# Kernel tuning notes

Measured on AMD Instinct MI355X. Metric: run time of the kernel, lower is better.

## Reference

```python
import jax, jax.numpy as jnp
import numpy as np

N_NODES = 8192
GNN_DIM = 512
N_FEAT = 64
N_ITER = 4


def setup_inputs() -> dict:
    key = jax.random.key(0)
    ks = jax.random.split(key, 8)
    scale = 1.0 / np.sqrt(GNN_DIM)
    return {
        "labels": jax.random.normal(ks[0], (N_NODES, GNN_DIM), dtype=jnp.float32),
        "adj": jax.random.uniform(ks[1], (N_NODES, N_NODES), dtype=jnp.float32),
        "features": jax.random.normal(ks[2], (N_FEAT,), dtype=jnp.float32),
        "W_self": jax.random.normal(ks[3], (GNN_DIM, GNN_DIM), dtype=jnp.float32) * scale,
        "b_self": jax.random.normal(ks[4], (GNN_DIM,), dtype=jnp.float32) * scale,
        "W_neigh": jax.random.normal(ks[5], (GNN_DIM, GNN_DIM), dtype=jnp.float32) * scale,
        "W_fc": jax.random.normal(ks[6], (1, GNN_DIM + N_FEAT), dtype=jnp.float32) * scale,
        "b_fc": jax.random.normal(ks[7], (1,), dtype=jnp.float32) * scale,
    }


def reference(labels, adj, features, W_self, b_self, W_neigh, W_fc, b_fc):
    x = labels  # [N, D]
    for _ in range(N_ITER):
        acc = adj @ x                                   # [N, D] neighbor aggregation
        x = jax.nn.relu(x @ W_self.T + b_self + acc @ W_neigh.T)
    pooled = jnp.mean(x, axis=0)                        # [D]
    z = jnp.concatenate([pooled, features]) @ W_fc.T + b_fc  # [1]
    return jax.nn.sigmoid(z)
```

## Files before the change

kernel.cpp:

```cpp
#include <hip/hip_runtime.h>

typedef __bf16 bf16;
typedef bf16 bf16x8 __attribute__((ext_vector_type(8)));
typedef bf16 bf16x4 __attribute__((ext_vector_type(4)));
typedef float f32x4 __attribute__((ext_vector_type(4)));
typedef long longx2 __attribute__((ext_vector_type(2)));
typedef unsigned int u32;
typedef unsigned int u32x2 __attribute__((ext_vector_type(2)));
typedef unsigned char u8;
typedef unsigned long long u64;

constexpr int NN = 8192;
constexpr int DD = 512;
constexpr size_t PSZB = (size_t)NN * DD * 2;
constexpr size_t PSZE = (size_t)NN * DD;
constexpr int NS = 4;

static __device__ inline bf16x8 cvt8(const float* __restrict__ p) {
  f32x4 a = *(const f32x4*)p;
  f32x4 b = *(const f32x4*)(p + 4);
  bf16x8 r;
  r[0] = (bf16)a[0]; r[1] = (bf16)a[1]; r[2] = (bf16)a[2]; r[3] = (bf16)a[3];
  r[4] = (bf16)b[0]; r[5] = (bf16)b[1]; r[6] = (bf16)b[2]; r[7] = (bf16)b[3];
  return r;
}

static __device__ inline unsigned f32_to_e4m3(float x) {
  float a = fabsf(x);
  unsigned s = (__float_as_uint(x) >> 24) & 0x80u;
  if (!(a < 448.f)) a = 448.f;
  if (a < 0.015625f)
    return s | (unsigned)(int)__builtin_rintf(a * 512.f);
  int e = (int)((__float_as_uint(a) >> 23) & 0xFF) - 127;
  float mul = __uint_as_float((unsigned)(130 - e) << 23);
  int t = (int)__builtin_rintf(a * mul);
  return s | (unsigned)((e + 6) * 8 + t);
}

#define GLDS(g, l) __builtin_amdgcn_global_load_lds( \
    (const __attribute__((address_space(1))) unsigned int*)(const void*)(g), \
    (__attribute__((address_space(3))) unsigned int*)(void*)(l), 16, 0, 0)


__global__ __launch_bounds__(256) void convert_w_kernel(
    const float* __restrict__ a, const float* __restrict__ b,
    bf16* __restrict__ ao, bf16* __restrict__ bo, float* __restrict__ pooled) {
  int tid = (int)threadIdx.x;
  if (blockIdx.x == 0) {
    pooled[tid] = 0.f;
    pooled[tid + 256] = 0.f;
  }
  int i8 = ((int)blockIdx.x * 256 + tid) * 8;
  if (i8 < DD * DD) {
    *(bf16x8*)&ao[i8] = cvt8(a + i8);
  } else {
    int j = i8 - DD * DD;
    *(bf16x8*)&bo[j] = cvt8(b + j);
  }
}

__global__ __launch_bounds__(256) void convert_adj_kernel(
    const float* __restrict__ a, u8* __restrict__ o) {
  int i = (int)blockIdx.x * 256 + (int)threadIdx.x;
  int row  = i >> 10;
  int rem  = i & 1023;
  int g    = rem >> 3;
  int fq   = rem & 3;
  int h    = (rem >> 2) & 1;
  const float* p = a + (size_t)row * NN + g * 64 + h * 32 + fq * 8;
  f32x4 v0 = *(const f32x4*)p;
  f32x4 v1 = *(const f32x4*)(p + 4);
  u32 w0 = 0, w1 = 0;
  w0 = __builtin_amdgcn_cvt_pk_fp8_f32(v0[0], v0[1], w0, false);
  w0 = __builtin_amdgcn_cvt_pk_fp8_f32(v0[2], v0[3], w0, true);
  w1 = __builtin_amdgcn_cvt_pk_fp8_f32(v1[0], v1[1], w1, false);
  w1 = __builtin_amdgcn_cvt_pk_fp8_f32(v1[2], v1[3], w1, true);
  u32x2 w; w[0] = w0; w[1] = w1;
  *(u32x2*)(o + (size_t)row * NN + g * 64 + fq * 16 + h * 8) = w;
}

__global__ __launch_bounds__(256) void convert_x_kernel(
    const float* __restrict__ src, bf16* __restrict__ xb, u8* __restrict__ xbT8) {
  __shared__ __align__(16) float tile[64][68];
  const int tid = (int)threadIdx.x;
  const int r0 = (int)blockIdx.x * 64;
  const int c0 = (int)blockIdx.y * 64;
#pragma unroll
  for (int p = 0; p < 4; ++p) {
    int row = p * 16 + (tid >> 4);
    int col = (tid & 15) * 4;
    *(f32x4*)&tile[row][col] = *(const f32x4*)&src[(size_t)(r0 + row) * DD + c0 + col];
  }
  __syncthreads();
#pragma unroll
  for (int p = 0; p < 4; ++p) {
    int row = p * 16 + (tid >> 4);
    int col = (tid & 15) * 4;
    f32x4 v = *(const f32x4*)&tile[row][col];
    bf16x4 o;
    o[0] = (bf16)v[0]; o[1] = (bf16)v[1]; o[2] = (bf16)v[2]; o[3] = (bf16)v[3];
    *(bf16x4*)&xb[(size_t)(r0 + row) * DD + c0 + col] = o;
  }
  {
    int c = tid >> 2;
    int rp = (tid & 3) * 16;
    size_t base = (size_t)(c0 + c) * NN + r0;
#pragma unroll
    for (int b = 0; b < 2; ++b) {
      u32 lo = 0, hi = 0;
      lo = __builtin_amdgcn_cvt_pk_fp8_f32(tile[rp + 8 * b + 0][c], tile[rp + 8 * b + 1][c], lo, false);
      lo = __builtin_amdgcn_cvt_pk_fp8_f32(tile[rp + 8 * b + 2][c], tile[rp + 8 * b + 3][c], lo, true);
      hi = __builtin_amdgcn_cvt_pk_fp8_f32(tile[rp + 8 * b + 4][c], tile[rp + 8 * b + 5][c], hi, false);
      hi = __builtin_amdgcn_cvt_pk_fp8_f32(tile[rp + 8 * b + 6][c], tile[rp + 8 * b + 7][c], hi, true);
      int u = (rp >> 3) + b;
      u32x2 w; w[0] = lo; w[1] = hi;
      *(u32x2*)&xbT8[base + (u & 3) * 16 + (u >> 2) * 8] = w;
    }
  }
}


__device__ __forceinline__ void stage_half8(const u8* __restrict__ g, int grow0, int k0b,
                                            u8* smbase, int wave, int lane) {
  int row = grow0 + wave * 16 + (lane >> 2);
  int col = k0b + (((lane & 3) ^ ((lane >> 2) & 3)) << 4);
  GLDS(g + (size_t)row * NN + col, smbase + wave * 1024);
}

__global__ __launch_bounds__(512, 2)
void gemm1_kernel(const u8* __restrict__ adjb, const u8* __restrict__ xbT8,
                  bf16* __restrict__ pbase) {
  __shared__ __align__(16) u8 sm[65536];
  const int bid  = (int)blockIdx.x;
  const int xcd  = bid & 7, ii = bid >> 3;
  const int cb   = ii & 1;
  const int jj_  = xcd + 8 * (ii >> 1);
  const int p    = jj_ >> 2;
  const int s    = jj_ & 3;
  const int prow0 = p * 256;
  const int bcol0 = cb * 256;
  const int kb    = s * 2048;
  bf16* __restrict__ P = pbase + (size_t)s * PSZE;

  const int tid  = (int)threadIdx.x;
  const int lane = tid & 63;
  const int wave = tid >> 6;
  const int wr   = wave >> 2;
  const int wc   = wave & 3;
  const int fr   = lane & 15, fq = lane >> 4;

  f32x4 acc[8][4] = {};

#define A_OFF(par) ((par) * 32768)
#define B_OFF(par) ((par) * 32768 + 16384)
#define STAGE_A(tile, half, par) \
  stage_half8(adjb, prow0 + (half) * 128, kb + ((tile) & 31) * 64, \
              sm + A_OFF(par) + (half) * 8192, wave, lane)
#define STAGE_B(tile, half, par) \
  stage_half8(xbT8, bcol0 + (half) * 128, kb + ((tile) & 31) * 64, \
              sm + B_OFF(par) + (half) * 8192, wave, lane)

  STAGE_B(0, 0, 0); STAGE_B(0, 1, 0); STAGE_A(0, 0, 0);
  STAGE_A(0, 1, 0); STAGE_B(1, 0, 1); STAGE_B(1, 1, 1); STAGE_A(1, 0, 1);

  longx2 bvp[4], afp[2];

#define LOAD_B(par)                                                        \
  _Pragma("unroll") for (int n = 0; n < 4; ++n) {                          \
    int rowl = wc * 64 + n * 16 + fr;                                      \
    int slot = fq ^ (rowl & 3);                                            \
    bvp[n] = *(const longx2*)&sm[B_OFF(par) + rowl * 64 + slot * 16];      \
  }
#define LOAD_A(q, par)                                                     \
  _Pragma("unroll") for (int j = 0; j < 2; ++j) {                          \
    int rowl = (q) * 64 + wr * 32 + j * 16 + fr;                           \
    int slot = fq ^ (rowl & 3);                                            \
    afp[j] = *(const longx2*)&sm[A_OFF(par) + rowl * 64 + slot * 16];      \
  }
#define QMFMA(q)                                                           \
  _Pragma("unroll") for (int kk = 0; kk < 2; ++kk)                         \
  _Pragma("unroll") for (int j = 0; j < 2; ++j)                            \
  _Pragma("unroll") for (int n = 0; n < 4; ++n)                            \
    acc[2 * (q) + j][n] = __builtin_amdgcn_mfma_f32_16x16x32_fp8_fp8(      \
        kk ? afp[j].y : afp[j].x, kk ? bvp[n].y : bvp[n].x,                \
        acc[2 * (q) + j][n], 0, 0, 0);
#define PHASE_TAIL(q)                                                      \
  __builtin_amdgcn_s_barrier();                                            \
  asm volatile("s_waitcnt lgkmcnt(0)" ::: "memory");                       \
  __builtin_amdgcn_sched_barrier(0);                                       \
  __builtin_amdgcn_s_setprio(1);                                           \
  QMFMA(q);                                                                \
  __builtin_amdgcn_s_setprio(0);                                           \
  __builtin_amdgcn_s_barrier();

  for (int it = 0; it < 16; ++it) {
    const int t = it * 2;
    asm volatile("s_waitcnt vmcnt(4)" ::: "memory");
    LOAD_B(0);
    LOAD_A(0, 0);
    STAGE_A(t + 1, 1, 1);
    PHASE_TAIL(0);
    LOAD_A(1, 0);
    STAGE_B(t + 2, 0, 0);
    PHASE_TAIL(1);
    asm volatile("s_waitcnt vmcnt(5)" ::: "memory");
    LOAD_A(2, 0);
    STAGE_B(t + 2, 1, 0);
    PHASE_TAIL(2);
    LOAD_A(3, 0);
    STAGE_A(t + 2, 0, 0);
    PHASE_TAIL(3);
    asm volatile("s_waitcnt vmcnt(4)" ::: "memory");
    LOAD_B(1);
    LOAD_A(0, 1);
    STAGE_A(t + 2, 1, 0);
    PHASE_TAIL(0);
    LOAD_A(1, 1);
    STAGE_B(t + 3, 0, 1);
    PHASE_TAIL(1);
    asm volatile("s_waitcnt vmcnt(5)" ::: "memory");
    LOAD_A(2, 1);
    STAGE_B(t + 3, 1, 1);
    PHASE_TAIL(2);
    LOAD_A(3, 1);
    STAGE_A(t + 3, 0, 1);
    PHASE_TAIL(3);
  }

#pragma unroll
  for (int m = 0; m < 8; ++m)
#pragma unroll
    for (int n = 0; n < 4; ++n)
#pragma unroll
      for (int r = 0; r < 4; ++r) {
        int row = prow0 + (m >> 1) * 64 + wr * 32 + (m & 1) * 16 + fq * 4 + r;
        int col = bcol0 + wc * 64 + n * 16 + fr;
        P[(size_t)row * DD + col] = (bf16)acc[m][n][r];
      }
#undef A_OFF
#undef B_OFF
#undef STAGE_A
#undef STAGE_B
#undef LOAD_B
#undef LOAD_A
#undef QMFMA
#undef PHASE_TAIL
}

__global__ __launch_bounds__(1024, 4)
void gemm2_kernel(const bf16* __restrict__ wsb, const bf16* __restrict__ wnb,
                  bf16* __restrict__ xb, const bf16* __restrict__ pbase,
                  const float* __restrict__ bself, u8* __restrict__ xbT8,
                  float* __restrict__ pooled, int dopool,
                  float alpha, float inv_an) {
  __shared__ __align__(16) char smem[139264];
  const int tid  = (int)threadIdx.x;
  const int lane = tid & 63;
  const int wave = tid >> 6;
  const int n0 = (int)blockIdx.x * 32;
  const int fr = lane & 15, fq = lane >> 4;
  const int srow = lane >> 3;
  const int scol = ((lane & 7) ^ (srow & 7)) * 8;
  const int fnode = tid >> 3, fks = tid & 7;

  f32x4 acc[2][2] = {};

  {
    bf16* la = (bf16*)smem;
#pragma unroll
    for (int c = 0; c < 4; ++c) {
      int chunk = wave * 4 + c;
      GLDS(wsb + (size_t)(chunk * 8 + srow) * DD + scol, &la[chunk * 512]);
    }
    if (wave < 4)
      GLDS(xb + (size_t)(n0 + wave * 8 + srow) * DD + scol,
           &((bf16*)(smem + 131072))[wave * 512]);
  }
  asm volatile("s_waitcnt vmcnt(0)" ::: "memory");
  __builtin_amdgcn_s_barrier();

  for (int t = 0; t < 16; ++t) {
    const int par = t & 1;
    bf16* la = (bf16*)(smem + par * 65536);
    bf16* lb = (bf16*)(smem + 131072 + par * 4096);

    bf16x8 fv0, fv1, fv2, fv3;
    bool fold = false;
    if (t < 15) {
      const int tn = t + 1, prn = tn >> 3, k0n = (tn & 7) * 64;
      const bf16* __restrict__ An = prn ? wnb : wsb;
      bf16* lan = (bf16*)(smem + (par ^ 1) * 65536);
#pragma unroll
      for (int c = 0; c < 4; ++c) {
        int chunk = wave * 4 + c;
        GLDS(An + (size_t)(chunk * 8 + srow) * DD + k0n + scol, &lan[chunk * 512]);
      }
      if (prn == 0) {
        if (wave < 4)
          GLDS(xb + (size_t)(n0 + wave * 8 + srow) * DD + k0n + scol,
               &((bf16*)(smem + 131072 + (par ^ 1) * 4096))[wave * 512]);
      } else if (tid < 256) {
        fold = true;
        const bf16* p0 = pbase + (size_t)(n0 + fnode) * DD + k0n + fks * 8;
        fv0 = *(const bf16x8*)(p0);
        fv1 = *(const bf16x8*)(p0 + PSZE);
        fv2 = *(const bf16x8*)(p0 + 2 * PSZE);
        fv3 = *(const bf16x8*)(p0 + 3 * PSZE);
      }
    }

    bf16x8 af[2][2], bv[2][2];
#pragma unroll
    for (int kk = 0; kk < 2; ++kk) {
#pragma unroll
      for (int m = 0; m < 2; ++m) {
        int rowl = wave * 32 + m * 16 + fr;
        int slot = (kk * 4 + fq) ^ (rowl & 7);
        af[kk][m] = *(const bf16x8*)&la[rowl * 64 + slot * 8];
      }
#pragma unroll
      for (int n = 0; n < 2; ++n) {
        int rowl = n * 16 + fr;
        int slot = (kk * 4 + fq) ^ (rowl & 7);
        bv[kk][n] = *(const bf16x8*)&lb[rowl * 64 + slot * 8];
      }
    }
#pragma unroll
    for (int kk = 0; kk < 2; ++kk)
#pragma unroll
      for (int m = 0; m < 2; ++m)
#pragma unroll
        for (int n = 0; n < 2; ++n)
          acc[m][n] = __builtin_amdgcn_mfma_f32_16x16x32_bf16(af[kk][m], bv[kk][n], acc[m][n], 0, 0, 0);

    if (fold) {
      bf16x8 o;
#pragma unroll
      for (int j = 0; j < 8; ++j)
        o[j] = (bf16)(((float)fv0[j] + (float)fv1[j] + (float)fv2[j] + (float)fv3[j]) * alpha);
      *(bf16x8*)&((bf16*)(smem + 131072 + (par ^ 1) * 4096))[fnode * 64 + (fks ^ (fnode & 7)) * 8] = o;
    }

    asm volatile("s_waitcnt vmcnt(0) lgkmcnt(0)" ::: "memory");
    __builtin_amdgcn_s_barrier();
  }

  bf16* lds_t = (bf16*)smem;
  u8*   lds8  = (u8*)(smem + 40960);
#pragma unroll
  for (int m = 0; m < 2; ++m)
#pragma unroll
    for (int n = 0; n < 2; ++n)
#pragma unroll
      for (int r = 0; r < 4; ++r) {
        int d = wave * 32 + m * 16 + fq * 4 + r;
        int node = n * 16 + fr;
        float v = acc[m][n][r] + bself[d];
        v = v > 0.f ? v : 0.f;
        lds_t[node * 520 + d] = (bf16)v;
        lds8[d * 32 + node] = (u8)f32_to_e4m3(v * inv_an);
      }
  if (dopool) {
#pragma unroll
    for (int m = 0; m < 2; ++m)
#pragma unroll
      for (int r = 0; r < 4; ++r) {
        int d = wave * 32 + m * 16 + fq * 4 + r;
        float b = bself[d];
        float v0 = acc[m][0][r] + b, v1 = acc[m][1][r] + b;
        float sv = (v0 > 0.f ? v0 : 0.f) + (v1 > 0.f ? v1 : 0.f);
        sv += __shfl_xor(sv, 1);
        sv += __shfl_xor(sv, 2);
        sv += __shfl_xor(sv, 4);
        sv += __shfl_xor(sv, 8);
        if (fr == 0) atomicAdd(&pooled[d], sv);
      }
  }
  __syncthreads();
  {
    int node = tid >> 5;
    int dc = (tid & 31) * 16;
    bf16x8 v0 = *(const bf16x8*)&lds_t[node * 520 + dc];
    bf16x8 v1 = *(const bf16x8*)&lds_t[node * 520 + dc + 8];
    *(bf16x8*)&xb[(size_t)(n0 + node) * DD + dc] = v0;
    *(bf16x8*)&xb[(size_t)(n0 + node) * DD + dc + 8] = v1;
  }
  {
    int d = tid >> 1, half = tid & 1;
    const u64* src = (const u64*)&lds8[d * 32 + half * 16];
    u64 w0 = src[0], w1 = src[1];
    size_t base = (size_t)d * NN + (size_t)(n0 & ~63) + ((n0 >> 5) & 1) * 8;
    *(u64*)&xbT8[base + half * 32] = w0;
    *(u64*)&xbT8[base + half * 32 + 16] = w1;
  }
}


__global__ __launch_bounds__(64) void final_kernel(
    const float* __restrict__ pooled, const float* __restrict__ features,
    const float* __restrict__ wfc, const float* __restrict__ bfc,
    float* __restrict__ out) {
  const int t = (int)threadIdx.x;
  float s = 0.f;
  for (int i = t; i < DD + 64; i += 64) {
    float v = (i < DD) ? pooled[i] * (1.0f / (float)NN) : features[i - DD];
    s += v * wfc[i];
  }
#pragma unroll
  for (int off = 32; off > 0; off >>= 1) s += __shfl_down(s, off);
  if (t == 0) {
    float z = s + bfc[0];
    out[0] = 1.0f / (1.0f + expf(-z));
  }
}


extern "C" void kernel_launch(void* const* d_in, const int* in_sizes, int n_in,
                              void* d_out, int out_size, void* d_ws, size_t ws_size,
                              hipStream_t stream) {
  const float* labels   = (const float*)d_in[0];
  const float* adj      = (const float*)d_in[1];
  const float* features = (const float*)d_in[2];
  const float* W_self   = (const float*)d_in[3];
  const float* b_self   = (const float*)d_in[4];
  const float* W_neigh  = (const float*)d_in[5];
  const float* W_fc     = (const float*)d_in[6];
  const float* b_fc     = (const float*)d_in[7];
  float* out = (float*)d_out;

  const float AL[5] = {1.f, 4.f, 2048.f, 4194304.f, 1.f};

  char* ws = (char*)d_ws;
  bf16*  xb    = (bf16*)(ws);
  u8*    xbT8  = (u8*)(ws + PSZB);
  bf16*  pbase = (bf16*)(ws + 2 * PSZB);
  char*  after_p = ws + (size_t)(2 + NS) * PSZB;
  bf16*  wsb    = (bf16*)(after_p);
  bf16*  wnb    = (bf16*)(after_p + 524288);
  float* pooled = (float*)(after_p + 1048576);
  u8*    adjb8  = (u8*)(after_p + 1048576 + 4096);

  convert_w_kernel<<<2 * DD * DD / 8 / 256, 256, 0, stream>>>(W_self, W_neigh, wsb, wnb, pooled);
  convert_adj_kernel<<<(int)((size_t)NN * NN / 8 / 256), 256, 0, stream>>>(adj, adjb8);
  convert_x_kernel<<<dim3(NN / 64, DD / 64), 256, 0, stream>>>(labels, xb, xbT8);

  for (int it = 0; it < 4; ++it) {
    gemm1_kernel<<<256, 512, 0, stream>>>(adjb8, xbT8, pbase);
    gemm2_kernel<<<NN / 32, 1024, 0, stream>>>(wsb, wnb, xb, pbase, b_self, xbT8,
                                               pooled, it == 3 ? 1 : 0,
                                               AL[it], 1.f / AL[it + 1]);
  }

  final_kernel<<<1, 64, 0, stream>>>(pooled, features, W_fc, b_fc, out);
}
```

Baseline: 412.6 us.

## Switch adjacency GEMM to 16x16x128 scaled FP8 MFMA with K=128 tiles

```diff
diff --git a/kernel.cpp b/kernel.cpp
--- a/kernel.cpp
+++ b/kernel.cpp
@@ -4,9 +4,11 @@
 typedef bf16 bf16x8 __attribute__((ext_vector_type(8)));
 typedef bf16 bf16x4 __attribute__((ext_vector_type(4)));
 typedef float f32x4 __attribute__((ext_vector_type(4)));
-typedef long longx2 __attribute__((ext_vector_type(2)));
+typedef int i32x4 __attribute__((ext_vector_type(4)));
+typedef int i32x8 __attribute__((ext_vector_type(8)));
 typedef unsigned int u32;
 typedef unsigned int u32x2 __attribute__((ext_vector_type(2)));
+typedef unsigned int u32x4 __attribute__((ext_vector_type(4)));
 typedef unsigned char u8;
 typedef unsigned long long u64;
 
@@ -15,6 +17,7 @@
 constexpr size_t PSZB = (size_t)NN * DD * 2;
 constexpr size_t PSZE = (size_t)NN * DD;
 constexpr int NS = 4;
+#define SC1 0x7F7F7F7Fu
 
 static __device__ inline bf16x8 cvt8(const float* __restrict__ p) {
   f32x4 a = *(const f32x4*)p;
@@ -61,22 +64,16 @@
 
 __global__ __launch_bounds__(256) void convert_adj_kernel(
     const float* __restrict__ a, u8* __restrict__ o) {
-  int i = (int)blockIdx.x * 256 + (int)threadIdx.x;
-  int row  = i >> 10;
-  int rem  = i & 1023;
-  int g    = rem >> 3;
-  int fq   = rem & 3;
-  int h    = (rem >> 2) & 1;
-  const float* p = a + (size_t)row * NN + g * 64 + h * 32 + fq * 8;
-  f32x4 v0 = *(const f32x4*)p;
-  f32x4 v1 = *(const f32x4*)(p + 4);
+  size_t i8 = ((size_t)blockIdx.x * 256 + threadIdx.x) * 8;
+  f32x4 v0 = *(const f32x4*)(a + i8);
+  f32x4 v1 = *(const f32x4*)(a + i8 + 4);
   u32 w0 = 0, w1 = 0;
   w0 = __builtin_amdgcn_cvt_pk_fp8_f32(v0[0], v0[1], w0, false);
   w0 = __builtin_amdgcn_cvt_pk_fp8_f32(v0[2], v0[3], w0, true);
   w1 = __builtin_amdgcn_cvt_pk_fp8_f32(v1[0], v1[1], w1, false);
   w1 = __builtin_amdgcn_cvt_pk_fp8_f32(v1[2], v1[3], w1, true);
   u32x2 w; w[0] = w0; w[1] = w1;
-  *(u32x2*)(o + (size_t)row * NN + g * 64 + fq * 16 + h * 8) = w;
+  *(u32x2*)(o + i8) = w;
 }
 
 __global__ __launch_bounds__(256) void convert_x_kernel(
@@ -104,33 +101,34 @@
   {
     int c = tid >> 2;
     int rp = (tid & 3) * 16;
-    size_t base = (size_t)(c0 + c) * NN + r0;
-#pragma unroll
-    for (int b = 0; b < 2; ++b) {
-      u32 lo = 0, hi = 0;
-      lo = __builtin_amdgcn_cvt_pk_fp8_f32(tile[rp + 8 * b + 0][c], tile[rp + 8 * b + 1][c], lo, false);
-      lo = __builtin_amdgcn_cvt_pk_fp8_f32(tile[rp + 8 * b + 2][c], tile[rp + 8 * b + 3][c], lo, true);
-      hi = __builtin_amdgcn_cvt_pk_fp8_f32(tile[rp + 8 * b + 4][c], tile[rp + 8 * b + 5][c], hi, false);
-      hi = __builtin_amdgcn_cvt_pk_fp8_f32(tile[rp + 8 * b + 6][c], tile[rp + 8 * b + 7][c], hi, true);
-      int u = (rp >> 3) + b;
-      u32x2 w; w[0] = lo; w[1] = hi;
-      *(u32x2*)&xbT8[base + (u & 3) * 16 + (u >> 2) * 8] = w;
+    u32x4 w;
+#pragma unroll
+    for (int q = 0; q < 4; ++q) {
+      u32 x = 0;
+      x = __builtin_amdgcn_cvt_pk_fp8_f32(tile[rp + 4 * q + 0][c], tile[rp + 4 * q + 1][c], x, false);
+      x = __builtin_amdgcn_cvt_pk_fp8_f32(tile[rp + 4 * q + 2][c], tile[rp + 4 * q + 3][c], x, true);
+      w[q] = x;
     }
-  }
-}
-
-
-__device__ __forceinline__ void stage_half8(const u8* __restrict__ g, int grow0, int k0b,
-                                            u8* smbase, int wave, int lane) {
-  int row = grow0 + wave * 16 + (lane >> 2);
-  int col = k0b + (((lane & 3) ^ ((lane >> 2) & 3)) << 4);
-  GLDS(g + (size_t)row * NN + col, smbase + wave * 1024);
+    *(u32x4*)&xbT8[(size_t)(c0 + c) * NN + r0 + rp] = w;
+  }
+}
+
+
+__device__ __forceinline__ void stage_half16(const u8* __restrict__ g, int grow0, int k0b,
+                                             u8* smbase, int wave, int lane) {
+#pragma unroll
+  for (int i = 0; i < 2; ++i) {
+    int c = wave * 2 + i;
+    int row = grow0 + c * 8 + (lane >> 3);
+    int col = k0b + (((lane & 7) ^ ((lane >> 3) & 7)) << 4);
+    GLDS(g + (size_t)row * NN + col, smbase + c * 1024);
+  }
 }
 
 __global__ __launch_bounds__(512, 2)
 void gemm1_kernel(const u8* __restrict__ adjb, const u8* __restrict__ xbT8,
                   bf16* __restrict__ pbase) {
-  __shared__ __align__(16) u8 sm[65536];
+  __shared__ __align__(16) u8 sm[131072];
   const int bid  = (int)blockIdx.x;
   const int xcd  = bid & 7, ii = bid >> 3;
   const int cb   = ii & 1;
@@ -151,51 +149,53 @@
 
   f32x4 acc[8][4] = {};
 
-#define A_OFF(par) ((par) * 32768)
-#define B_OFF(par) ((par) * 32768 + 16384)
+#define A_OFF(par) ((par) * 65536)
+#define B_OFF(par) ((par) * 65536 + 32768)
 #define STAGE_A(tile, half, par) \
-  stage_half8(adjb, prow0 + (half) * 128, kb + ((tile) & 31) * 64, \
-              sm + A_OFF(par) + (half) * 8192, wave, lane)
+  stage_half16(adjb, prow0 + (half) * 128, kb + ((tile) & 15) * 128, \
+               sm + A_OFF(par) + (half) * 16384, wave, lane)
 #define STAGE_B(tile, half, par) \
-  stage_half8(xbT8, bcol0 + (half) * 128, kb + ((tile) & 31) * 64, \
-              sm + B_OFF(par) + (half) * 8192, wave, lane)
+  stage_half16(xbT8, bcol0 + (half) * 128, kb + ((tile) & 15) * 128, \
+               sm + B_OFF(par) + (half) * 16384, wave, lane)
 
   STAGE_B(0, 0, 0); STAGE_B(0, 1, 0); STAGE_A(0, 0, 0);
   STAGE_A(0, 1, 0); STAGE_B(1, 0, 1); STAGE_B(1, 1, 1); STAGE_A(1, 0, 1);
 
-  longx2 bvp[4], afp[2];
-
-#define LOAD_B(par)                                                        \
-  _Pragma("unroll") for (int n = 0; n < 4; ++n) {                          \
-    int rowl = wc * 64 + n * 16 + fr;                                      \
-    int slot = fq ^ (rowl & 3);                                            \
-    bvp[n] = *(const longx2*)&sm[B_OFF(par) + rowl * 64 + slot * 16];      \
-  }
-#define LOAD_A(q, par)                                                     \
-  _Pragma("unroll") for (int j = 0; j < 2; ++j) {                          \
-    int rowl = (q) * 64 + wr * 32 + j * 16 + fr;                           \
-    int slot = fq ^ (rowl & 3);                                            \
-    afp[j] = *(const longx2*)&sm[A_OFF(par) + rowl * 64 + slot * 16];      \
-  }
-#define QMFMA(q)                                                           \
-  _Pragma("unroll") for (int kk = 0; kk < 2; ++kk)                         \
-  _Pragma("unroll") for (int j = 0; j < 2; ++j)                            \
-  _Pragma("unroll") for (int n = 0; n < 4; ++n)                            \
-    acc[2 * (q) + j][n] = __builtin_amdgcn_mfma_f32_16x16x32_fp8_fp8(      \
-        kk ? afp[j].y : afp[j].x, kk ? bvp[n].y : bvp[n].x,                \
-        acc[2 * (q) + j][n], 0, 0, 0);
-#define PHASE_TAIL(q)                                                      \
-  __builtin_amdgcn_s_barrier();                                            \
-  asm volatile("s_waitcnt lgkmcnt(0)" ::: "memory");                       \
-  __builtin_amdgcn_sched_barrier(0);                                       \
-  __builtin_amdgcn_s_setprio(1);                                           \
-  QMFMA(q);                                                                \
-  __builtin_amdgcn_s_setprio(0);                                           \
+  i32x8 bvp[4], afp[2];
+
+#define LOAD_B(par)                                                          \
+  _Pragma("unroll") for (int n = 0; n < 4; ++n) {                            \
+    int rowl = wc * 64 + n * 16 + fr;                                        \
+    const u8* rb = &sm[B_OFF(par) + rowl * 128];                             \
+    i32x4 lo = *(const i32x4*)&rb[((2 * fq) ^ (rowl & 7)) * 16];             \
+    i32x4 hi = *(const i32x4*)&rb[((2 * fq + 1) ^ (rowl & 7)) * 16];         \
+    bvp[n] = __builtin_shufflevector(lo, hi, 0, 1, 2, 3, 4, 5, 6, 7);        \
+  }
+#define LOAD_A(q, par)                                                       \
+  _Pragma("unroll") for (int j = 0; j < 2; ++j) {                            \
+    int rowl = (q) * 64 + wr * 32 + j * 16 + fr;                             \
+    const u8* ra = &sm[A_OFF(par) + rowl * 128];                             \
+    i32x4 lo = *(const i32x4*)&ra[((2 * fq) ^ (rowl & 7)) * 16];             \
+    i32x4 hi = *(const i32x4*)&ra[((2 * fq + 1) ^ (rowl & 7)) * 16];         \
+    afp[j] = __builtin_shufflevector(lo, hi, 0, 1, 2, 3, 4, 5, 6, 7);        \
+  }
+#define QMFMA(q)                                                             \
+  _Pragma("unroll") for (int j = 0; j < 2; ++j)                              \
+  _Pragma("unroll") for (int n = 0; n < 4; ++n)                              \
+    acc[2 * (q) + j][n] = __builtin_amdgcn_mfma_scale_f32_16x16x128_f8f6f4(  \
+        afp[j], bvp[n], acc[2 * (q) + j][n], 0, 0, 0, SC1, 0, SC1);
+#define PHASE_TAIL(q)                                                        \
+  __builtin_amdgcn_s_barrier();                                              \
+  asm volatile("s_waitcnt lgkmcnt(0)" ::: "memory");                         \
+  __builtin_amdgcn_sched_barrier(0);                                         \
+  __builtin_amdgcn_s_setprio(1);                                             \
+  QMFMA(q);                                                                  \
+  __builtin_amdgcn_s_setprio(0);                                             \
   __builtin_amdgcn_s_barrier();
 
-  for (int it = 0; it < 16; ++it) {
+  for (int it = 0; it < 8; ++it) {
     const int t = it * 2;
-    asm volatile("s_waitcnt vmcnt(4)" ::: "memory");
+    asm volatile("s_waitcnt vmcnt(8)" ::: "memory");
     LOAD_B(0);
     LOAD_A(0, 0);
     STAGE_A(t + 1, 1, 1);
@@ -203,14 +203,14 @@
     LOAD_A(1, 0);
     STAGE_B(t + 2, 0, 0);
     PHASE_TAIL(1);
-    asm volatile("s_waitcnt vmcnt(5)" ::: "memory");
+    asm volatile("s_waitcnt vmcnt(10)" ::: "memory");
     LOAD_A(2, 0);
     STAGE_B(t + 2, 1, 0);
     PHASE_TAIL(2);
     LOAD_A(3, 0);
     STAGE_A(t + 2, 0, 0);
     PHASE_TAIL(3);
-    asm volatile("s_waitcnt vmcnt(4)" ::: "memory");
+    asm volatile("s_waitcnt vmcnt(8)" ::: "memory");
     LOAD_B(1);
     LOAD_A(0, 1);
     STAGE_A(t + 2, 1, 0);
@@ -218,7 +218,7 @@
     LOAD_A(1, 1);
     STAGE_B(t + 3, 0, 1);
     PHASE_TAIL(1);
-    asm volatile("s_waitcnt vmcnt(5)" ::: "memory");
+    asm volatile("s_waitcnt vmcnt(10)" ::: "memory");
     LOAD_A(2, 1);
     STAGE_B(t + 3, 1, 1);
     PHASE_TAIL(2);
@@ -387,11 +387,8 @@
   }
   {
     int d = tid >> 1, half = tid & 1;
-    const u64* src = (const u64*)&lds8[d * 32 + half * 16];
-    u64 w0 = src[0], w1 = src[1];
-    size_t base = (size_t)d * NN + (size_t)(n0 & ~63) + ((n0 >> 5) & 1) * 8;
-    *(u64*)&xbT8[base + half * 32] = w0;
-    *(u64*)&xbT8[base + half * 32 + 16] = w1;
+    u32x4 w = *(const u32x4*)&lds8[d * 32 + half * 16];
+    *(u32x4*)&xbT8[(size_t)d * NN + n0 + half * 16] = w;
   }
 }
 
```

Result: slower. 499.8 us (+21.1%).
